# Kernel optimization log

Hardware: AMD Instinct MI355X
Metric: run time of the kernel (lower is better)

Reference implementation:

```python
import jax, jax.numpy as jnp
import numpy as np

DIM = 192; D_STATE = 16; D_CONV = 4; EXPAND = 2
D_INNER = EXPAND * DIM          # 384
DT_RANK = -(-DIM // 16)         # ceil(192/16) = 12
BSZ, T, H, W = 1, 16, 64, 64


def setup_inputs() -> dict:
    key = jax.random.key(0)
    ks = jax.random.split(key, 10)
    s = 0.02
    return {
        "x": jax.random.normal(ks[0], (BSZ, DIM, T, H, W), jnp.float32),
        "ln1_g": jnp.ones((DIM,), jnp.float32),
        "ln1_b": jnp.zeros((DIM,), jnp.float32),
        "ln2_g": jnp.ones((DIM,), jnp.float32),
        "ln2_b": jnp.zeros((DIM,), jnp.float32),
        "W_in": jax.random.normal(ks[1], (2 * D_INNER, DIM), jnp.float32) * s,
        "conv_w": jax.random.normal(ks[2], (D_INNER, D_CONV), jnp.float32) * 0.3,
        "conv_b": jnp.zeros((D_INNER,), jnp.float32),
        "W_xp": jax.random.normal(ks[3], (DT_RANK + 2 * D_STATE, D_INNER), jnp.float32) * s,
        "W_dt": jax.random.normal(ks[4], (D_INNER, DT_RANK), jnp.float32) * 0.1,
        "b_dt": jax.random.normal(ks[5], (D_INNER,), jnp.float32) * 0.1 - 4.0,
        "A_log": jnp.log(jnp.broadcast_to(jnp.arange(1, D_STATE + 1, dtype=jnp.float32), (D_INNER, D_STATE))),
        "D": jnp.ones((D_INNER,), jnp.float32),
        "W_out": jax.random.normal(ks[6], (DIM, D_INNER), jnp.float32) * s,
    }


def _layer_norm(x, g, b, eps=1e-5):
    m = x.mean(-1, keepdims=True)
    v = ((x - m) ** 2).mean(-1, keepdims=True)
    return (x - m) * jax.lax.rsqrt(v + eps) * g + b


def _mamba(tokens, W_in, conv_w, conv_b, W_xp, W_dt, b_dt, A_log, D, W_out):
    B, L, _ = tokens.shape
    xz = tokens @ W_in.T                      # (B, L, 2*d_inner)
    xc, z = jnp.split(xz, 2, axis=-1)
    # causal depthwise conv1d along L
    xin = xc.transpose(0, 2, 1)               # (B, d_inner, L)
    xconv = jax.lax.conv_general_dilated(
        xin, conv_w[:, None, :], (1,), [(D_CONV - 1, 0)],
        dimension_numbers=("NCH", "OIH", "NCH"), feature_group_count=D_INNER)
    xconv = xconv + conv_b[None, :, None]
    xs = jax.nn.silu(xconv.transpose(0, 2, 1))  # (B, L, d_inner)
    x_dbl = xs @ W_xp.T                        # (B, L, dt_rank + 2*d_state)
    dt, Bm, Cm = jnp.split(x_dbl, [DT_RANK, DT_RANK + D_STATE], axis=-1)
    dt = jax.nn.softplus(dt @ W_dt.T + b_dt)   # (B, L, d_inner)
    A = -jnp.exp(A_log)                        # (d_inner, d_state)
    dA = jnp.exp(dt[..., None] * A)            # (B, L, d_inner, d_state)
    dBx = dt[..., None] * Bm[:, :, None, :] * xs[..., None]

    def step(h, inp):
        dA_t, dBx_t, C_t = inp
        h = dA_t * h + dBx_t                   # (B, d_inner, d_state)
        return h, jnp.einsum("bds,bs->bd", h, C_t)

    h0 = jnp.zeros((B, D_INNER, D_STATE), tokens.dtype)
    _, ys = jax.lax.scan(step, h0, (dA.transpose(1, 0, 2, 3),
                                    dBx.transpose(1, 0, 2, 3),
                                    Cm.transpose(1, 0, 2)))
    y = ys.transpose(1, 0, 2) + xs * D         # (B, L, d_inner)
    y = y * jax.nn.silu(z)
    return y @ W_out.T                          # (B, L, dim)


def reference(x, ln1_g, ln1_b, ln2_g, ln2_b, W_in, conv_w, conv_b,
              W_xp, W_dt, b_dt, A_log, D, W_out):
    B, C, T_, H_, W_ = x.shape
    Hs, Ws = H_ // 4, W_ // 4
    # avg_pool3d kernel=(1,4,4) stride=(1,4,4)
    x_ds = x.reshape(B, C, T_, Hs, 4, Ws, 4).mean((4, 6))
    tokens = x_ds.reshape(B, C, T_ * Hs * Ws).transpose(0, 2, 1)  # (B, L, C)
    y = _layer_norm(tokens, ln1_g, ln1_b)
    y = _mamba(y, W_in, conv_w, conv_b, W_xp, W_dt, b_dt, A_log, D, W_out)
    out = _layer_norm(tokens + y, ln2_g, ln2_b)                    # (B, L, C)
    out5 = out.transpose(0, 2, 1).reshape(B, C, T_, Hs, Ws)
    pooled = out5.mean((3, 4))                                     # (B, C, T)
    mag = jnp.abs(jnp.fft.rfft(pooled, axis=2))
    weight = jax.nn.sigmoid(mag[:, :, 1:8].mean(-1))               # (B, C)
    out5 = out5 * weight[:, :, None, None, None]
    up = jax.image.resize(out5, (B, C, T_, H_, W_), method="trilinear")
    return up * jax.nn.sigmoid(x)
```

## Files before the change

### kernel.cpp

```cpp
#include <hip/hip_runtime.h>
#include <math.h>

#define DIMC 192
#define DI   384
#define DS   16
#define LTOK 4096
#define NCH  256
#define CLEN 16
#define NLANE (DI*DS)
#define L2E  1.4426950408889634f
#define LN2  0.6931471805599453f

typedef __attribute__((ext_vector_type(8))) short    bf16x8;
typedef __attribute__((ext_vector_type(8))) unsigned short u16x8;
typedef __attribute__((ext_vector_type(4))) float    f32x4;

__device__ __forceinline__ float EXP2(float x) { return __builtin_amdgcn_exp2f(x); }
__device__ __forceinline__ float RCP(float x)  { return __builtin_amdgcn_rcpf(x); }
__device__ __forceinline__ float LOG2(float x) { return __builtin_amdgcn_logf(x); }

__device__ __forceinline__ float sigmoidf_(float x) { return RCP(1.f + EXP2(-x * L2E)); }
__device__ __forceinline__ float siluf_(float x)    { return x * RCP(1.f + EXP2(-x * L2E)); }
__device__ __forceinline__ unsigned short f2bf(float f) {
    unsigned int u = __float_as_uint(f);
    u += 0x7FFFu + ((u >> 16) & 1u);
    return (unsigned short)(u >> 16);
}
__device__ __forceinline__ float bf2f(unsigned short b) {
    return __uint_as_float(((unsigned int)b) << 16);
}

__global__ __launch_bounds__(256) void poolln_kernel(const float* __restrict__ x,
                                                     const float* __restrict__ g,
                                                     const float* __restrict__ bb,
                                                     const float* __restrict__ W_in,
                                                     const float* __restrict__ W_out,
                                                     const float* __restrict__ W_xp,
                                                     const float* __restrict__ A_log,
                                                     float* __restrict__ tokens,
                                                     unsigned short* __restrict__ ytok,
                                                     unsigned short* __restrict__ W_in_bf,
                                                     unsigned short* __restrict__ W_out_bf,
                                                     unsigned short* __restrict__ W_xp_pad,
                                                     float* __restrict__ A2pre) {
    int blk = blockIdx.x;
    int tid = threadIdx.x;
    if (blk >= 256) {
        int id = (blk - 256) * 256 + tid;
        for (int i = id; i < 768 * 192; i += 8192) W_in_bf[i] = f2bf(W_in[i]);
        for (int i = id; i < 192 * 384; i += 8192) W_out_bf[i] = f2bf(W_out[i]);
        for (int i = id; i < 64 * 384; i += 8192) {
            int row = i / 384;
            W_xp_pad[i] = (row < 44) ? f2bf(W_xp[i]) : (unsigned short)0;
        }
        for (int i = id; i < NLANE; i += 8192) A2pre[i] = -expf(A_log[i]) * L2E;
        return;
    }
    int t = blk >> 4, hs = blk & 15;
    int grp = tid >> 4, ws = tid & 15;
    __shared__ float P[16 * 196];
    __shared__ float ms[16], rs[16];
    #pragma unroll
    for (int k = 0; k < 12; ++k) {
        int c = grp + (k << 4);
        const float* base = x + ((size_t)(c * 16 + t) * 64 + hs * 4) * 64 + ws * 4;
        float s = 0.f;
        #pragma unroll
        for (int i = 0; i < 4; ++i) {
            float4 v = *(const float4*)(base + i * 64);
            s += v.x + v.y + v.z + v.w;
        }
        P[ws * 196 + c] = s * 0.0625f;
    }
    __syncthreads();
    float s1 = 0.f, s2 = 0.f;
    #pragma unroll
    for (int k = 0; k < 12; ++k) {
        float v = P[grp * 196 + ws + 16 * k];
        s1 += v; s2 += v * v;
    }
    s1 += __shfl_xor(s1, 1); s2 += __shfl_xor(s2, 1);
    s1 += __shfl_xor(s1, 2); s2 += __shfl_xor(s2, 2);
    s1 += __shfl_xor(s1, 4); s2 += __shfl_xor(s2, 4);
    s1 += __shfl_xor(s1, 8); s2 += __shfl_xor(s2, 8);
    if (ws == 0) {
        float m = s1 * (1.f / 192.f);
        ms[grp] = m;
        rs[grp] = rsqrtf(s2 * (1.f / 192.f) - m * m + 1e-5f);
    }
    __syncthreads();
    int l0 = t * 256 + hs * 16;
    for (int e = tid; e < 16 * 192; e += 256) {
        int w2 = e / 192, c = e - w2 * 192;
        float v = P[w2 * 196 + c];
        float val = (v - ms[w2]) * rs[w2] * g[c] + bb[c];
        tokens[(size_t)(l0 + w2) * DIMC + c] = v;
        ytok[(size_t)(l0 + w2) * DIMC + c] = f2bf(val);
    }
}

__global__ __launch_bounds__(256) void gemm_in(const unsigned short* __restrict__ A,
                                               const unsigned short* __restrict__ Wb,
                                               unsigned short* __restrict__ xcb,
                                               unsigned short* __restrict__ zsb) {
    constexpr int K = 192, KP = K + 8;
    __shared__ unsigned short As[64 * KP];
    __shared__ unsigned short Bs[64 * KP];
    int bm = blockIdx.y * 64;
    int bn = blockIdx.x * 64;
    int tid = threadIdx.x;
    int lane = tid & 63, w = tid >> 6;
    int wr = w >> 1, wc = w & 1;
    int r16 = lane & 15, h = lane >> 4;
    for (int c = tid; c < 64 * (K / 8); c += 256) {
        int row = c / (K / 8), col = (c % (K / 8)) * 8;
        *(u16x8*)&As[row * KP + col] = *(const u16x8*)(A + (size_t)(bm + row) * K + col);
        *(u16x8*)&Bs[row * KP + col] = *(const u16x8*)(Wb + (size_t)(bn + row) * K + col);
    }
    __syncthreads();
    f32x4 acc[2][2] = {};
    #pragma unroll
    for (int k0 = 0; k0 < K; k0 += 32) {
        bf16x8 a0 = *(const bf16x8*)&As[(wr * 32 + r16)      * KP + k0 + 8 * h];
        bf16x8 a1 = *(const bf16x8*)&As[(wr * 32 + 16 + r16) * KP + k0 + 8 * h];
        bf16x8 b0 = *(const bf16x8*)&Bs[(wc * 32 + r16)      * KP + k0 + 8 * h];
        bf16x8 b1 = *(const bf16x8*)&Bs[(wc * 32 + 16 + r16) * KP + k0 + 8 * h];
        acc[0][0] = __builtin_amdgcn_mfma_f32_16x16x32_bf16(a0, b0, acc[0][0], 0, 0, 0);
        acc[0][1] = __builtin_amdgcn_mfma_f32_16x16x32_bf16(a0, b1, acc[0][1], 0, 0, 0);
        acc[1][0] = __builtin_amdgcn_mfma_f32_16x16x32_bf16(a1, b0, acc[1][0], 0, 0, 0);
        acc[1][1] = __builtin_amdgcn_mfma_f32_16x16x32_bf16(a1, b1, acc[1][1], 0, 0, 0);
    }
    bool isz = (bn >= 384);
    #pragma unroll
    for (int fm = 0; fm < 2; ++fm)
        #pragma unroll
        for (int fn = 0; fn < 2; ++fn)
            #pragma unroll
            for (int i = 0; i < 4; ++i) {
                int r = bm + wr * 32 + fm * 16 + h * 4 + i;
                int cc = bn + wc * 32 + fn * 16 + r16;
                float v = acc[fm][fn][i];
                if (isz) zsb[(size_t)r * DI + (cc - 384)] = f2bf(siluf_(v));
                else     xcb[(size_t)r * DI + cc]         = f2bf(v);
            }
}

__global__ __launch_bounds__(256) void convxdbl(const unsigned short* __restrict__ xcb,
                                                const float* __restrict__ conv_w,
                                                const float* __restrict__ conv_b,
                                                const unsigned short* __restrict__ Wxp,
                                                unsigned short* __restrict__ xsb,
                                                float* __restrict__ x_dbl) {
    int l0 = blockIdx.x * 16;
    int tid = threadIdx.x;
    __shared__ unsigned short As[16 * 392];
    __shared__ float xd[16 * 64];
    for (int e = tid * 2; e < 16 * 384; e += 512) {
        int row = e / 384, d = e - row * 384;
        int l = l0 + row;
        float ax = conv_b[d], ay = conv_b[d + 1];
        #pragma unroll
        for (int k = 0; k < 4; ++k) {
            int ll = l - 3 + k;
            if (ll >= 0) {
                ushort2 u = *(const ushort2*)(xcb + (size_t)ll * DI + d);
                ax = fmaf(conv_w[d * 4 + k],       bf2f(u.x), ax);
                ay = fmaf(conv_w[(d + 1) * 4 + k], bf2f(u.y), ay);
            }
        }
        ushort2 b2;
        b2.x = f2bf(siluf_(ax));
        b2.y = f2bf(siluf_(ay));
        *(ushort2*)&As[row * 392 + d] = b2;
        *(ushort2*)(xsb + (size_t)l * 384 + d) = b2;
    }
    __syncthreads();
    int lane = tid & 63, w = tid >> 6;
    int r16 = lane & 15, hh = lane >> 4;
    f32x4 acc = {};
    #pragma unroll
    for (int k0 = 0; k0 < 384; k0 += 32) {
        bf16x8 a = *(const bf16x8*)&As[r16 * 392 + k0 + 8 * hh];
        bf16x8 b = *(const bf16x8*)(Wxp + (size_t)(w * 16 + r16) * 384 + k0 + 8 * hh);
        acc = __builtin_amdgcn_mfma_f32_16x16x32_bf16(a, b, acc, 0, 0, 0);
    }
    #pragma unroll
    for (int i = 0; i < 4; ++i) xd[(hh * 4 + i) * 64 + w * 16 + r16] = acc[i];
    __syncthreads();
    {
        int e = tid * 4;
        int row = e >> 6, col = e & 63;
        *(float4*)(x_dbl + (size_t)(l0 + row) * 64 + col) = *(const float4*)&xd[e];
    }
}

__global__ __launch_bounds__(256) void scan1(const float* __restrict__ x_dbl,
                                             const unsigned short* __restrict__ xsb,
                                             const float* __restrict__ W_dt,
                                             const float* __restrict__ b_dt,
                                             const float* __restrict__ A2pre,
                                             float* __restrict__ chA,
                                             float* __restrict__ chB,
                                             float* __restrict__ Dloc,
                                             unsigned short* __restrict__ yloc) {
    int tid = threadIdx.x;
    int dg = blockIdx.x;
    int c  = blockIdx.y;
    __shared__ float xdblS[16 * 48];
    __shared__ float wdtS[64 * 13];
    __shared__ float dtS[16][64];
    __shared__ unsigned short xsS[16][64];
    for (int i = tid; i < 768; i += 256) {
        int row = i / 48, col = i - row * 48;
        xdblS[i] = x_dbl[(size_t)(c * 16 + row) * 64 + col];
    }
    for (int i = tid; i < 768; i += 256) {
        int dl_ = i / 12, r = i - dl_ * 12;
        wdtS[dl_ * 13 + r] = W_dt[(size_t)dg * 768 + i];
    }
    for (int i = tid; i < 1024; i += 256) {
        int row = i >> 6, dl_ = i & 63;
        xsS[row][dl_] = xsb[(size_t)(c * 16 + row) * 384 + dg * 64 + dl_];
    }
    __syncthreads();
    {
        int dl_ = tid & 63;
        float bd = b_dt[dg * 64 + dl_];
        #pragma unroll
        for (int i2 = 0; i2 < 4; ++i2) {
            int row = (tid >> 6) + 4 * i2;
            float s = bd;
            #pragma unroll
            for (int r = 0; r < 12; ++r)
                s = fmaf(xdblS[row * 48 + r], wdtS[dl_ * 13 + r], s);
            dtS[row][dl_] = (s > 20.f) ? s : LOG2(1.f + EXP2(s * L2E)) * LN2;
        }
    }
    __syncthreads();
    int sq = tid & 3, dl = tid >> 2;
    int d = dg * 64 + dl;
    float4 a4 = *(const float4*)(A2pre + (size_t)d * DS + sq * 4);
    float A2[4] = {a4.x, a4.y, a4.z, a4.w};
    float h[4] = {};
    float dts = 0.f;
    #pragma unroll
    for (int i = 0; i < CLEN; ++i) {
        int l = c * CLEN + i;
        float dtv = dtS[i][dl];
        float xv  = bf2f(xsS[i][dl]);
        float dtx = dtv * xv;
        dts += dtv;
        float y = 0.f;
        #pragma unroll
        for (int u = 0; u < 4; ++u) {
            float a = EXP2(dtv * A2[u]);
            h[u] = fmaf(a, h[u], dtx * xdblS[i * 48 + 12 + sq * 4 + u]);
            y = fmaf(h[u], xdblS[i * 48 + 28 + sq * 4 + u], y);
        }
        y += __shfl_xor(y, 1);
        y += __shfl_xor(y, 2);
        if (sq == 0) {
            yloc[(size_t)l * DI + d] = f2bf(y);
            Dloc[(size_t)l * DI + d] = dts;
        }
    }
    size_t base = (size_t)c * NLANE + d * DS + sq * 4;
    float4 pa, pb;
    pa.x = EXP2(dts * A2[0]); pa.y = EXP2(dts * A2[1]);
    pa.z = EXP2(dts * A2[2]); pa.w = EXP2(dts * A2[3]);
    pb.x = h[0]; pb.y = h[1]; pb.z = h[2]; pb.w = h[3];
    *(float4*)&chA[base] = pa;
    *(float4*)&chB[base] = pb;
}

__global__ __launch_bounds__(256) void scan2p(const float* __restrict__ chA,
                                              const float* __restrict__ chB,
                                              float* __restrict__ hst) {
    int tid = threadIdx.x;
    int ll = tid & 15;
    int g  = tid >> 4;
    int lane = blockIdx.x * 16 + ll;
    float a[16], b[16];
    #pragma unroll
    for (int i = 0; i < 16; ++i) {
        int c = g * 16 + i;
        a[i] = chA[(size_t)c * NLANE + lane];
        b[i] = chB[(size_t)c * NLANE + lane];
    }
    float Ath = 1.f, Bth = 0.f;
    #pragma unroll
    for (int i = 0; i < 16; ++i) {
        Bth = fmaf(a[i], Bth, b[i]);
        Ath *= a[i];
    }
    __shared__ float sA[16][17], sB[16][17];
    sA[g][ll] = Ath; sB[g][ll] = Bth;
    __syncthreads();
    #pragma unroll
    for (int step = 1; step < 16; step <<= 1) {
        float pA = 1.f, pB = 0.f;
        if (g >= step) { pA = sA[g - step][ll]; pB = sB[g - step][ll]; }
        __syncthreads();
        if (g >= step) {
            float cA = sA[g][ll], cB = sB[g][ll];
            sA[g][ll] = cA * pA;
            sB[g][ll] = fmaf(cA, pB, cB);
        }
        __syncthreads();
    }
    float h = (g == 0) ? 0.f : sB[g - 1][ll];
    #pragma unroll
    for (int i = 0; i < 16; ++i) {
        int c = g * 16 + i;
        hst[(size_t)c * NLANE + lane] = h;
        h = fmaf(a[i], h, b[i]);
    }
}

__global__ __launch_bounds__(512) void gemmscanln(const float* __restrict__ hst,
                                                  const float* __restrict__ Dloc,
                                                  const float* __restrict__ x_dbl,
                                                  const float* __restrict__ A2pre,
                                                  const unsigned short* __restrict__ yloc,
                                                  const unsigned short* __restrict__ xsb,
                                                  const unsigned short* __restrict__ zsb,
                                                  const float* __restrict__ Dvec,
                                                  const unsigned short* __restrict__ Wb,
                                                  const float* __restrict__ tokens,
                                                  const float* __restrict__ g,
                                                  const float* __restrict__ bb,
                                                  float* __restrict__ o5) {
    constexpr int K = 384, KT = 96, KP = KT + 8;
    __shared__ unsigned short ybufS[16 * 392];
    __shared__ char smem2[192 * KP * 2];
    unsigned short* Bs = (unsigned short*)smem2;
    float* P = (float*)smem2;
    __shared__ float hpS[2][16 * 17];
    __shared__ float A2S[2][16 * 17];
    __shared__ float CsS[256];
    __shared__ float ms[16], rs[16];
    int c = blockIdx.x;
    int tid = threadIdx.x;
    int half = tid >> 8, t8 = tid & 255;
    int ll = t8 >> 4, sl = t8 & 15;
    if (tid < 256) CsS[tid] = x_dbl[(size_t)(c * 16 + (tid >> 4)) * 64 + 28 + (tid & 15)];
    int l = c * 16 + ll;
    for (int dgi = 0; dgi < 12; ++dgi) {
        int dg = dgi * 2 + half;
        hpS[half][ll * 17 + sl] = hst[(size_t)c * NLANE + dg * 256 + t8];
        A2S[half][ll * 17 + sl] = A2pre[(size_t)dg * 256 + t8];
        __syncthreads();
        int d = dg * 16 + sl;
        float Dl = Dloc[(size_t)l * DI + d];
        float y  = bf2f(yloc[(size_t)l * DI + d]);
        float xv = bf2f(xsb[(size_t)l * DI + d]);
        float zs = bf2f(zsb[(size_t)l * DI + d]);
        #pragma unroll
        for (int s = 0; s < 16; ++s) {
            float e = EXP2(A2S[half][sl * 17 + s] * Dl);
            y = fmaf(CsS[ll * 16 + s] * e, hpS[half][sl * 17 + s], y);
        }
        float val = (y + xv * Dvec[d]) * zs;
        ybufS[ll * 392 + d] = f2bf(val);
        __syncthreads();
    }
    int lane = tid & 63, w = tid >> 6;
    int r16 = lane & 15, hh = lane >> 4;
    f32x4 acc0 = {}, acc1 = {};
    for (int kt = 0; kt < K; kt += KT) {
        for (int cc2 = tid; cc2 < 192 * 12; cc2 += 512) {
            int row = cc2 / 12, col = (cc2 % 12) * 8;
            *(u16x8*)&Bs[row * KP + col] = *(const u16x8*)(Wb + (size_t)row * K + kt + col);
        }
        __syncthreads();
        #pragma unroll
        for (int k0 = 0; k0 < KT; k0 += 32) {
            bf16x8 a = *(const bf16x8*)&ybufS[r16 * 392 + kt + k0 + 8 * hh];
            bf16x8 b0 = *(const bf16x8*)&Bs[(w * 16 + r16) * KP + k0 + 8 * hh];
            acc0 = __builtin_amdgcn_mfma_f32_16x16x32_bf16(a, b0, acc0, 0, 0, 0);
            if (w < 4) {
                bf16x8 b1 = *(const bf16x8*)&Bs[((8 + w) * 16 + r16) * KP + k0 + 8 * hh];
                acc1 = __builtin_amdgcn_mfma_f32_16x16x32_bf16(a, b1, acc1, 0, 0, 0);
            }
        }
        __syncthreads();
    }
    for (int e = tid; e < 16 * 192; e += 512) {
        int row = e / 192, col = e - row * 192;
        P[row * 193 + col] = tokens[(size_t)(c * 16 + row) * DIMC + col];
    }
    __syncthreads();
    #pragma unroll
    for (int i = 0; i < 4; ++i)
        P[(hh * 4 + i) * 193 + w * 16 + r16] += acc0[i];
    if (w < 4)
        #pragma unroll
        for (int i = 0; i < 4; ++i)
            P[(hh * 4 + i) * 193 + (8 + w) * 16 + r16] += acc1[i];
    __syncthreads();
    {
        int tk = tid >> 5, q = tid & 31;
        float s1 = 0.f, s2 = 0.f;
        #pragma unroll
        for (int u = 0; u < 6; ++u) {
            float v = P[tk * 193 + q * 6 + u];
            s1 += v; s2 += v * v;
        }
        s1 += __shfl_xor(s1, 1);  s2 += __shfl_xor(s2, 1);
        s1 += __shfl_xor(s1, 2);  s2 += __shfl_xor(s2, 2);
        s1 += __shfl_xor(s1, 4);  s2 += __shfl_xor(s2, 4);
        s1 += __shfl_xor(s1, 8);  s2 += __shfl_xor(s2, 8);
        s1 += __shfl_xor(s1, 16); s2 += __shfl_xor(s2, 16);
        if (q == 0) {
            float m = s1 * (1.f / 192.f);
            ms[tk] = m;
            rs[tk] = rsqrtf(s2 * (1.f / 192.f) - m * m + 1e-5f);
        }
    }
    __syncthreads();
    int t = c >> 4;
    int sp0 = (c * 16) & 255;
    for (int e = tid; e < 16 * 192; e += 512) {
        int cch = e >> 4, row = e & 15;
        float val = (P[row * 193 + cch] - ms[row]) * rs[row] * g[cch] + bb[cch];
        o5[(size_t)cch * 4096 + t * 256 + sp0 + row] = val;
    }
}

__global__ __launch_bounds__(256) void upfft(const float* __restrict__ o5,
                                             const float* __restrict__ x,
                                             float* __restrict__ out) {
    int blk = blockIdx.x;
    int c = blk >> 4, t = blk & 15;
    int tid = threadIdx.x;
    __shared__ float pl[256];
    __shared__ float pooled[16];
    __shared__ float mag[8];
    __shared__ float wgt_s;
    int wv = tid >> 6, lane = tid & 63;
    #pragma unroll
    for (int rr = 0; rr < 4; ++rr) {
        int r = wv * 4 + rr;
        float s = 0.f;
        #pragma unroll
        for (int u = 0; u < 4; ++u) {
            float v = o5[(size_t)c * 4096 + r * 256 + lane + u * 64];
            s += v;
            if (r == t) pl[lane + u * 64] = v;
        }
        s += __shfl_xor(s, 1); s += __shfl_xor(s, 2); s += __shfl_xor(s, 4);
        s += __shfl_xor(s, 8); s += __shfl_xor(s, 16); s += __shfl_xor(s, 32);
        if (lane == 0) pooled[r] = s * (1.f / 256.f);
    }
    __syncthreads();
    if (tid >= 1 && tid <= 7) {
        int k = tid;
        float re = 0.f, im = 0.f;
        for (int tt = 0; tt < 16; ++tt) {
            float ang = -0.39269908169872414f * (float)(k * tt);
            re = fmaf(pooled[tt], __cosf(ang), re);
            im = fmaf(pooled[tt], __sinf(ang), im);
        }
        mag[k] = sqrtf(re * re + im * im);
    }
    __syncthreads();
    if (tid == 0) {
        float m = 0.f;
        for (int k = 1; k <= 7; ++k) m += mag[k];
        wgt_s = sigmoidf_(m * (1.f / 7.f));
    }
    __syncthreads();
    float wc = wgt_s;
    size_t planeoff = (size_t)blk * 4096;
    #pragma unroll
    for (int p = 0; p < 4; ++p) {
        int px4 = p * 256 + tid;
        int k = px4 & 15;
        int hrow = px4 >> 4;
        float sh = hrow * 0.25f - 0.375f;
        int h0 = (int)floorf(sh); float fh = sh - (float)h0;
        int h0c = min(max(h0, 0), 15), h1c = min(max(h0 + 1, 0), 15);
        int cm = max(k - 1, 0), cp = min(k + 1, 15);
        float r0m = pl[h0c * 16 + cm], r00 = pl[h0c * 16 + k], r0p = pl[h0c * 16 + cp];
        float r1m = pl[h1c * 16 + cm], r10 = pl[h1c * 16 + k], r1p = pl[h1c * 16 + cp];
        float gh = 1.f - fh;
        float vm = r0m * gh + r1m * fh;
        float v0 = r00 * gh + r10 * fh;
        float vp = r0p * gh + r1p * fh;
        size_t off = planeoff + (size_t)px4 * 4;
        float4 xv = *(const float4*)(x + off);
        float4 o;
        o.x = (vm * 0.375f + v0 * 0.625f) * wc * sigmoidf_(xv.x);
        o.y = (vm * 0.125f + v0 * 0.875f) * wc * sigmoidf_(xv.y);
        o.z = (v0 * 0.875f + vp * 0.125f) * wc * sigmoidf_(xv.z);
        o.w = (v0 * 0.625f + vp * 0.375f) * wc * sigmoidf_(xv.w);
        *(float4*)(out + off) = o;
    }
}

extern "C" void kernel_launch(void* const* d_in, const int* in_sizes, int n_in,
                              void* d_out, int out_size, void* d_ws, size_t ws_size,
                              hipStream_t stream) {
    const float* x      = (const float*)d_in[0];
    const float* ln1_g  = (const float*)d_in[1];
    const float* ln1_b  = (const float*)d_in[2];
    const float* ln2_g  = (const float*)d_in[3];
    const float* ln2_b  = (const float*)d_in[4];
    const float* W_in   = (const float*)d_in[5];
    const float* conv_w = (const float*)d_in[6];
    const float* conv_b = (const float*)d_in[7];
    const float* W_xp   = (const float*)d_in[8];
    const float* W_dt   = (const float*)d_in[9];
    const float* b_dt   = (const float*)d_in[10];
    const float* A_log  = (const float*)d_in[11];
    const float* Dvec   = (const float*)d_in[12];
    const float* W_out  = (const float*)d_in[13];
    float* out = (float*)d_out;

    float* ws = (float*)d_ws;
    float* tokens = ws;  ws += (size_t)LTOK * DIMC;
    float* x_dbl  = ws;  ws += (size_t)LTOK * 64;
    float* chA    = ws;  ws += (size_t)NLANE * NCH;
    float* chB    = ws;  ws += (size_t)NLANE * NCH;
    float* hst    = ws;  ws += (size_t)NLANE * NCH;
    float* Dloc   = ws;  ws += (size_t)LTOK * DI;
    float* o5     = ws;  ws += (size_t)DIMC * LTOK;
    float* A2pre  = ws;  ws += NLANE;
    unsigned short* ytok     = (unsigned short*)ws;  ws += (size_t)LTOK * DIMC / 2;
    unsigned short* yloc     = (unsigned short*)ws;  ws += (size_t)LTOK * DI / 2;
    unsigned short* xsb      = (unsigned short*)ws;  ws += (size_t)LTOK * DI / 2;
    unsigned short* xcb      = (unsigned short*)ws;  ws += (size_t)LTOK * DI / 2;
    unsigned short* zsb      = (unsigned short*)ws;  ws += (size_t)LTOK * DI / 2;
    unsigned short* W_in_bf  = (unsigned short*)ws;  ws += (size_t)768 * 192 / 2;
    unsigned short* W_out_bf = (unsigned short*)ws;  ws += (size_t)192 * 384 / 2;
    unsigned short* W_xp_pad = (unsigned short*)ws;  ws += (size_t)64 * 384 / 2;

    poolln_kernel<<<288, 256, 0, stream>>>(x, ln1_g, ln1_b, W_in, W_out, W_xp, A_log,
                                           tokens, ytok, W_in_bf, W_out_bf, W_xp_pad, A2pre);
    gemm_in<<<dim3(12, 64), 256, 0, stream>>>(ytok, W_in_bf, xcb, zsb);
    convxdbl<<<256, 256, 0, stream>>>(xcb, conv_w, conv_b, W_xp_pad, xsb, x_dbl);
    scan1<<<dim3(6, NCH), 256, 0, stream>>>(x_dbl, xsb, W_dt, b_dt, A2pre, chA, chB, Dloc, yloc);
    scan2p<<<NLANE / 16, 256, 0, stream>>>(chA, chB, hst);
    gemmscanln<<<256, 512, 0, stream>>>(hst, Dloc, x_dbl, A2pre, yloc, xsb, zsb, Dvec,
                                        W_out_bf, tokens, ln2_g, ln2_b, o5);
    upfft<<<3072, 256, 0, stream>>>(o5, x, out);
}
```

Baseline: 110.9 us.

## Fuse temporal pooling into LN2 epilogue, halve scan chunks, store tokens as bf16

```diff
diff --git a/kernel.cpp b/kernel.cpp
--- a/kernel.cpp
+++ b/kernel.cpp
@@ -5,8 +5,8 @@
 #define DI   384
 #define DS   16
 #define LTOK 4096
-#define NCH  256
-#define CLEN 16
+#define NCH  128
+#define CLEN 32
 #define NLANE (DI*DS)
 #define L2E  1.4426950408889634f
 #define LN2  0.6931471805599453f
@@ -37,12 +37,13 @@
                                                      const float* __restrict__ W_out,
                                                      const float* __restrict__ W_xp,
                                                      const float* __restrict__ A_log,
-                                                     float* __restrict__ tokens,
+                                                     unsigned short* __restrict__ tokb,
                                                      unsigned short* __restrict__ ytok,
                                                      unsigned short* __restrict__ W_in_bf,
                                                      unsigned short* __restrict__ W_out_bf,
                                                      unsigned short* __restrict__ W_xp_pad,
-                                                     float* __restrict__ A2pre) {
+                                                     float* __restrict__ A2pre,
+                                                     float* __restrict__ pooled) {
     int blk = blockIdx.x;
     int tid = threadIdx.x;
     if (blk >= 256) {
@@ -54,6 +55,7 @@
             W_xp_pad[i] = (row < 44) ? f2bf(W_xp[i]) : (unsigned short)0;
         }
         for (int i = id; i < NLANE; i += 8192) A2pre[i] = -expf(A_log[i]) * L2E;
+        for (int i = id; i < 192 * 16; i += 8192) pooled[i] = 0.f;
         return;
     }
     int t = blk >> 4, hs = blk & 15;
@@ -94,7 +96,7 @@
         int w2 = e / 192, c = e - w2 * 192;
         float v = P[w2 * 196 + c];
         float val = (v - ms[w2]) * rs[w2] * g[c] + bb[c];
-        tokens[(size_t)(l0 + w2) * DIMC + c] = v;
+        tokb[(size_t)(l0 + w2) * DIMC + c] = f2bf(v);
         ytok[(size_t)(l0 + w2) * DIMC + c] = f2bf(val);
     }
 }
@@ -206,28 +208,28 @@
     int tid = threadIdx.x;
     int dg = blockIdx.x;
     int c  = blockIdx.y;
-    __shared__ float xdblS[16 * 48];
+    __shared__ float xdblS[CLEN * 48];
     __shared__ float wdtS[64 * 13];
-    __shared__ float dtS[16][64];
-    __shared__ unsigned short xsS[16][64];
-    for (int i = tid; i < 768; i += 256) {
+    __shared__ float dtS[CLEN][64];
+    __shared__ unsigned short xsS[CLEN][64];
+    for (int i = tid; i < CLEN * 48; i += 256) {
         int row = i / 48, col = i - row * 48;
-        xdblS[i] = x_dbl[(size_t)(c * 16 + row) * 64 + col];
+        xdblS[i] = x_dbl[(size_t)(c * CLEN + row) * 64 + col];
     }
     for (int i = tid; i < 768; i += 256) {
         int dl_ = i / 12, r = i - dl_ * 12;
         wdtS[dl_ * 13 + r] = W_dt[(size_t)dg * 768 + i];
     }
-    for (int i = tid; i < 1024; i += 256) {
+    for (int i = tid; i < CLEN * 64; i += 256) {
         int row = i >> 6, dl_ = i & 63;
-        xsS[row][dl_] = xsb[(size_t)(c * 16 + row) * 384 + dg * 64 + dl_];
+        xsS[row][dl_] = xsb[(size_t)(c * CLEN + row) * 384 + dg * 64 + dl_];
     }
     __syncthreads();
     {
         int dl_ = tid & 63;
         float bd = b_dt[dg * 64 + dl_];
         #pragma unroll
-        for (int i2 = 0; i2 < 4; ++i2) {
+        for (int i2 = 0; i2 < CLEN / 4; ++i2) {
             int row = (tid >> 6) + 4 * i2;
             float s = bd;
             #pragma unroll
@@ -277,9 +279,9 @@
                                               const float* __restrict__ chB,
                                               float* __restrict__ hst) {
     int tid = threadIdx.x;
-    int ll = tid & 15;
-    int g  = tid >> 4;
-    int lane = blockIdx.x * 16 + ll;
+    int ll = tid & 31;
+    int g  = tid >> 5;
+    int lane = blockIdx.x * 32 + ll;
     float a[16], b[16];
     #pragma unroll
     for (int i = 0; i < 16; ++i) {
@@ -293,11 +295,11 @@
         Bth = fmaf(a[i], Bth, b[i]);
         Ath *= a[i];
     }
-    __shared__ float sA[16][17], sB[16][17];
+    __shared__ float sA[8][33], sB[8][33];
     sA[g][ll] = Ath; sB[g][ll] = Bth;
     __syncthreads();
     #pragma unroll
-    for (int step = 1; step < 16; step <<= 1) {
+    for (int step = 1; step < 8; step <<= 1) {
         float pA = 1.f, pB = 0.f;
         if (g >= step) { pA = sA[g - step][ll]; pB = sB[g - step][ll]; }
         __syncthreads();
@@ -326,10 +328,11 @@
                                                   const unsigned short* __restrict__ zsb,
                                                   const float* __restrict__ Dvec,
                                                   const unsigned short* __restrict__ Wb,
-                                                  const float* __restrict__ tokens,
+                                                  const unsigned short* __restrict__ tokb,
                                                   const float* __restrict__ g,
                                                   const float* __restrict__ bb,
-                                                  float* __restrict__ o5) {
+                                                  float* __restrict__ o5,
+                                                  float* __restrict__ pooled) {
     constexpr int K = 384, KT = 96, KP = KT + 8;
     __shared__ unsigned short ybufS[16 * 392];
     __shared__ char smem2[192 * KP * 2];
@@ -340,6 +343,7 @@
     __shared__ float CsS[256];
     __shared__ float ms[16], rs[16];
     int c = blockIdx.x;
+    int c32 = c >> 1;
     int tid = threadIdx.x;
     int half = tid >> 8, t8 = tid & 255;
     int ll = t8 >> 4, sl = t8 & 15;
@@ -347,7 +351,7 @@
     int l = c * 16 + ll;
     for (int dgi = 0; dgi < 12; ++dgi) {
         int dg = dgi * 2 + half;
-        hpS[half][ll * 17 + sl] = hst[(size_t)c * NLANE + dg * 256 + t8];
+        hpS[half][ll * 17 + sl] = hst[(size_t)c32 * NLANE + dg * 256 + t8];
         A2S[half][ll * 17 + sl] = A2pre[(size_t)dg * 256 + t8];
         __syncthreads();
         int d = dg * 16 + sl;
@@ -387,7 +391,7 @@
     }
     for (int e = tid; e < 16 * 192; e += 512) {
         int row = e / 192, col = e - row * 192;
-        P[row * 193 + col] = tokens[(size_t)(c * 16 + row) * DIMC + col];
+        P[row * 193 + col] = bf2f(tokb[(size_t)(c * 16 + row) * DIMC + col]);
     }
     __syncthreads();
     #pragma unroll
@@ -424,42 +428,32 @@
         int cch = e >> 4, row = e & 15;
         float val = (P[row * 193 + cch] - ms[row]) * rs[row] * g[cch] + bb[cch];
         o5[(size_t)cch * 4096 + t * 256 + sp0 + row] = val;
+        float s = val;
+        s += __shfl_xor(s, 1); s += __shfl_xor(s, 2);
+        s += __shfl_xor(s, 4); s += __shfl_xor(s, 8);
+        if (row == 0) atomicAdd(&pooled[cch * 16 + t], s);
     }
 }
 
 __global__ __launch_bounds__(256) void upfft(const float* __restrict__ o5,
+                                             const float* __restrict__ pooled,
                                              const float* __restrict__ x,
                                              float* __restrict__ out) {
     int blk = blockIdx.x;
     int c = blk >> 4, t = blk & 15;
     int tid = threadIdx.x;
     __shared__ float pl[256];
-    __shared__ float pooled[16];
     __shared__ float mag[8];
     __shared__ float wgt_s;
-    int wv = tid >> 6, lane = tid & 63;
-    #pragma unroll
-    for (int rr = 0; rr < 4; ++rr) {
-        int r = wv * 4 + rr;
-        float s = 0.f;
-        #pragma unroll
-        for (int u = 0; u < 4; ++u) {
-            float v = o5[(size_t)c * 4096 + r * 256 + lane + u * 64];
-            s += v;
-            if (r == t) pl[lane + u * 64] = v;
-        }
-        s += __shfl_xor(s, 1); s += __shfl_xor(s, 2); s += __shfl_xor(s, 4);
-        s += __shfl_xor(s, 8); s += __shfl_xor(s, 16); s += __shfl_xor(s, 32);
-        if (lane == 0) pooled[r] = s * (1.f / 256.f);
-    }
-    __syncthreads();
+    pl[tid] = o5[(size_t)c * 4096 + t * 256 + tid];
     if (tid >= 1 && tid <= 7) {
         int k = tid;
         float re = 0.f, im = 0.f;
         for (int tt = 0; tt < 16; ++tt) {
+            float pv = pooled[c * 16 + tt] * (1.f / 256.f);
             float ang = -0.39269908169872414f * (float)(k * tt);
-            re = fmaf(pooled[tt], __cosf(ang), re);
-            im = fmaf(pooled[tt], __sinf(ang), im);
+            re = fmaf(pv, __cosf(ang), re);
+            im = fmaf(pv, __sinf(ang), im);
         }
         mag[k] = sqrtf(re * re + im * im);
     }
@@ -518,7 +512,6 @@
     float* out = (float*)d_out;
 
     float* ws = (float*)d_ws;
-    float* tokens = ws;  ws += (size_t)LTOK * DIMC;
     float* x_dbl  = ws;  ws += (size_t)LTOK * 64;
     float* chA    = ws;  ws += (size_t)NLANE * NCH;
     float* chB    = ws;  ws += (size_t)NLANE * NCH;
@@ -526,6 +519,8 @@
     float* Dloc   = ws;  ws += (size_t)LTOK * DI;
     float* o5     = ws;  ws += (size_t)DIMC * LTOK;
     float* A2pre  = ws;  ws += NLANE;
+    float* pooled = ws;  ws += 192 * 16;
+    unsigned short* tokb     = (unsigned short*)ws;  ws += (size_t)LTOK * DIMC / 2;
     unsigned short* ytok     = (unsigned short*)ws;  ws += (size_t)LTOK * DIMC / 2;
     unsigned short* yloc     = (unsigned short*)ws;  ws += (size_t)LTOK * DI / 2;
     unsigned short* xsb      = (unsigned short*)ws;  ws += (size_t)LTOK * DI / 2;
@@ -536,12 +531,12 @@
     unsigned short* W_xp_pad = (unsigned short*)ws;  ws += (size_t)64 * 384 / 2;
 
     poolln_kernel<<<288, 256, 0, stream>>>(x, ln1_g, ln1_b, W_in, W_out, W_xp, A_log,
-                                           tokens, ytok, W_in_bf, W_out_bf, W_xp_pad, A2pre);
+                                           tokb, ytok, W_in_bf, W_out_bf, W_xp_pad, A2pre, pooled);
     gemm_in<<<dim3(12, 64), 256, 0, stream>>>(ytok, W_in_bf, xcb, zsb);
     convxdbl<<<256, 256, 0, stream>>>(xcb, conv_w, conv_b, W_xp_pad, xsb, x_dbl);
     scan1<<<dim3(6, NCH), 256, 0, stream>>>(x_dbl, xsb, W_dt, b_dt, A2pre, chA, chB, Dloc, yloc);
-    scan2p<<<NLANE / 16, 256, 0, stream>>>(chA, chB, hst);
+    scan2p<<<NLANE / 32, 256, 0, stream>>>(chA, chB, hst);
     gemmscanln<<<256, 512, 0, stream>>>(hst, Dloc, x_dbl, A2pre, yloc, xsb, zsb, Dvec,
-                                        W_out_bf, tokens, ln2_g, ln2_b, o5);
-    upfft<<<3072, 256, 0, stream>>>(o5, x, out);
-}
+                                        W_out_bf, tokb, ln2_g, ln2_b, o5, pooled);
+    upfft<<<3072, 256, 0, stream>>>(o5, pooled, x, out);
+}
```

Result: slower. 114.1 us (+2.9%).
